# Kernel tuning notes

Hardware: AMD Instinct MI355X
Metric: run time of the kernel (lower is better)

The kernel has to match this reference:

```python
import jax, jax.numpy as jnp
import numpy as np

B, P, K = 32, 1024, 16  # clouds, points per cloud, neighbors


def setup_inputs() -> dict:
    key = jax.random.key(0)
    ks = jax.random.split(key, 5)
    N, C, H, D = B * P, 64, 128, 3
    x = jax.random.normal(ks[0], (N, C), dtype=jnp.float32)
    pos = jax.random.normal(ks[1], (N, D), dtype=jnp.float32)
    batch = jnp.arange(N, dtype=jnp.int64) // P  # cloud id per node
    W_e = jax.random.normal(ks[2], (2 * C, H), dtype=jnp.float32) * 0.05
    b_e = jnp.zeros((H,), dtype=jnp.float32)
    W_sc = jax.random.normal(ks[3], (C, H), dtype=jnp.float32) * 0.05
    b_sc = jnp.zeros((H,), dtype=jnp.float32)
    return {"x": x, "pos": pos, "batch": batch,
            "W_e": W_e, "b_e": b_e, "W_sc": W_sc, "b_sc": b_sc}


def _knn_idx(posb):
    # posb: [B, P, D] -> idx [B, P, K]: K nearest neighbors (sources) per target node,
    # within each cloud, excluding self (loop=False in torch_geometric.knn_graph).
    sq = jnp.sum(posb * posb, axis=-1)                       # [B, P]
    d2 = sq[:, :, None] + sq[:, None, :] - 2.0 * jnp.einsum('bid,bjd->bij', posb, posb)
    d2 = d2 + jnp.eye(P, dtype=posb.dtype)[None] * jnp.finfo(posb.dtype).max / 2
    _, idx = jax.lax.top_k(-d2, K)                           # [B, P, K]
    return idx


def reference(x, pos, batch, W_e, b_e, W_sc, b_sc):
    C = x.shape[-1]
    xb = x.reshape(B, P, C)
    posb = pos.reshape(B, P, -1)
    idx = _knn_idx(posb)                                     # [B, P, K]
    # gather neighbor (source) features per target node
    x_j = jax.vmap(lambda xc, ic: xc[ic])(xb, idx)           # [B, P, K, C]
    x_i = xb[:, :, None, :]                                  # [B, P, 1, C]
    # EdgeConv message: nn([x_i, x_j - x_i]), here Linear + ReLU
    e = jnp.concatenate([jnp.broadcast_to(x_i, x_j.shape), x_j - x_i], axis=-1)  # [B,P,K,2C]
    msg = jax.nn.relu(jnp.einsum('bpke,eh->bpkh', e, W_e) + b_e)
    agg = jnp.max(msg, axis=2)                               # max aggregation -> [B, P, H]
    shortcut = x @ W_sc + b_sc                               # [N, H]
    out = agg.reshape(-1, agg.shape[-1]) + shortcut
    return out
```

## Files before the change

### kernel.cpp

```cpp
#include <hip/hip_runtime.h>
#include <float.h>
#include <stdint.h>

#define BATCHES 32
#define P 1024
#define KNN 16
#define C 64
#define H 128
#define N (BATCHES * P)
#define NCOLS 384
#define SPLITS 8
#define CPS 128
#define PADH 132

typedef short short8 __attribute__((ext_vector_type(8)));
typedef float floatx4 __attribute__((ext_vector_type(4)));

__device__ __forceinline__ unsigned short f2bf(float f) {
    unsigned u = __float_as_uint(f);
    unsigned r = (u + 0x7FFF + ((u >> 16) & 1)) >> 16;
    return (unsigned short)r;
}

__global__ __launch_bounds__(256) void prep_w(
    const float* __restrict__ W_e, const float* __restrict__ b_e,
    const float* __restrict__ W_sc, const float* __restrict__ b_sc,
    unsigned short* __restrict__ WT, float* __restrict__ bias)
{
    int i = blockIdx.x * 256 + threadIdx.x;
    int col = i >> 6, c = i & 63;
    float w;
    if (col < 128)      w = W_e[c * 128 + col] - W_e[(64 + c) * 128 + col];
    else if (col < 256) w = W_e[(64 + c) * 128 + (col - 128)];
    else                w = W_sc[c * 128 + (col - 256)];
    WT[col * 64 + c] = f2bf(w);
    if (c == 0) {
        bias[col] = (col < 128) ? b_e[col] : (col < 256 ? 0.0f : b_sc[col - 256]);
    }
}

struct alignas(16) F4 { float x, y, z, w; };

struct PA {
    F4    spos[P];
    float lists[SPLITS][16][64];
    unsigned short elist[SPLITS][16][64];
    int   ecnt[SPLITS][64];
    float Tq[64];
};
struct PB {
    unsigned short Ubuf[64][PADH];
    unsigned short Vbuf[64][PADH];
    unsigned short Sbuf[64][PADH];
};

__global__ __launch_bounds__(512) void knn_gemm_kernel(
    const float* __restrict__ pos, const float* __restrict__ X,
    const unsigned short* __restrict__ WT, const float* __restrict__ bias,
    int* __restrict__ idx_out,
    unsigned short* __restrict__ U, unsigned short* __restrict__ V,
    unsigned short* __restrict__ S)
{
    __shared__ __align__(16) char smraw[sizeof(PA)];
    PA* A  = (PA*)smraw;
    PB* Bm = (PB*)smraw;

    int t = threadIdx.x;
    int q = t & 63, s = t >> 6;
    int blk = blockIdx.x;
    int batch = blk >> 4;
    int qblk  = blk & 15;
    int iloc  = qblk * 64 + q;

    const float* pb = pos + (size_t)batch * P * 3;
    for (int j = t; j < P; j += 512) {
        float x = pb[j * 3 + 0], y = pb[j * 3 + 1], z = pb[j * 3 + 2];
        float sq = __fadd_rn(__fadd_rn(__fmul_rn(x, x), __fmul_rn(y, y)),
                             __fmul_rn(z, z));
        A->spos[j] = F4{x, y, z, sq};
    }
    __syncthreads();

    F4 me = A->spos[iloc];
    float d[16];
#pragma unroll
    for (int k = 0; k < 16; ++k) d[k] = FLT_MAX;

    const int j0 = s * CPS;
#pragma unroll 4
    for (int jj = 0; jj < CPS; ++jj) {
        int j = j0 + jj;
        F4 c = A->spos[j];
        float dot = __fadd_rn(__fadd_rn(__fmul_rn(me.x, c.x), __fmul_rn(me.y, c.y)),
                              __fmul_rn(me.z, c.z));
        float d2 = __fadd_rn(__fadd_rn(me.w, c.w), __fmul_rn(-2.0f, dot));
        if (j == iloc) d2 = FLT_MAX;
#pragma unroll
        for (int k = 15; k >= 1; --k)
            d[k] = __builtin_amdgcn_fmed3f(d[k - 1], d2, d[k]);
        d[0] = fminf(d[0], d2);
    }
#pragma unroll
    for (int k = 0; k < 16; ++k) A->lists[s][k][q] = d[k];
    __syncthreads();

    if (s == 0) {
        float v0 = A->lists[0][0][q], v1 = A->lists[1][0][q];
        float v2 = A->lists[2][0][q], v3 = A->lists[3][0][q];
        float v4 = A->lists[4][0][q], v5 = A->lists[5][0][q];
        float v6 = A->lists[6][0][q], v7 = A->lists[7][0][q];
        int p0 = 0, p1 = 0, p2 = 0, p3 = 0, p4 = 0, p5 = 0, p6 = 0, p7 = 0;
        float T = 0.0f;
        for (int k = 0; k < 16; ++k) {
            float mn = fminf(fminf(fminf(v0, v1), fminf(v2, v3)),
                             fminf(fminf(v4, v5), fminf(v6, v7)));
            if      (v0 == mn) { p0++; v0 = (p0 < 16) ? A->lists[0][p0][q] : FLT_MAX; }
            else if (v1 == mn) { p1++; v1 = (p1 < 16) ? A->lists[1][p1][q] : FLT_MAX; }
            else if (v2 == mn) { p2++; v2 = (p2 < 16) ? A->lists[2][p2][q] : FLT_MAX; }
            else if (v3 == mn) { p3++; v3 = (p3 < 16) ? A->lists[3][p3][q] : FLT_MAX; }
            else if (v4 == mn) { p4++; v4 = (p4 < 16) ? A->lists[4][p4][q] : FLT_MAX; }
            else if (v5 == mn) { p5++; v5 = (p5 < 16) ? A->lists[5][p5][q] : FLT_MAX; }
            else if (v6 == mn) { p6++; v6 = (p6 < 16) ? A->lists[6][p6][q] : FLT_MAX; }
            else               { p7++; v7 = (p7 < 16) ? A->lists[7][p7][q] : FLT_MAX; }
            T = mn;
        }
        A->Tq[q] = T;
    }
    __syncthreads();
    float T = A->Tq[q];

    int cnt = 0;
    for (int jj = 0; jj < CPS; ++jj) {
        int j = j0 + jj;
        F4 c = A->spos[j];
        float dot = __fadd_rn(__fadd_rn(__fmul_rn(me.x, c.x), __fmul_rn(me.y, c.y)),
                              __fmul_rn(me.z, c.z));
        float d2 = __fadd_rn(__fadd_rn(me.w, c.w), __fmul_rn(-2.0f, dot));
        if (j == iloc) d2 = FLT_MAX;
        if (d2 <= T && cnt < 16) {
            A->elist[s][cnt][q] = (unsigned short)j;
            cnt++;
        }
    }
    A->ecnt[s][q] = cnt;
    __syncthreads();

    if (s == 0) {
        int o = 0;
        int base = batch * P;
        int gbase = (blk * 64 + q) * KNN;
#pragma unroll
        for (int ss = 0; ss < SPLITS; ++ss) {
            int cc = A->ecnt[ss][q];
            for (int k = 0; k < cc && o < KNN; ++k) {
                idx_out[gbase + o] = base + (int)A->elist[ss][k][q];
                o++;
            }
        }
    }
    __syncthreads();

    {
        int mt = s & 3, nh = s >> 2;
        int m0 = blk * 64 + mt * 16;
        int lm = q & 15, kg = q >> 4;

        const float4* arow = (const float4*)(X + (size_t)(m0 + lm) * 64 + kg * 8);
        float4 f0 = arow[0], f1 = arow[1];
        float4 f2 = arow[8], f3 = arow[9];
        short8 a0, a1;
        a0[0] = (short)f2bf(f0.x); a0[1] = (short)f2bf(f0.y);
        a0[2] = (short)f2bf(f0.z); a0[3] = (short)f2bf(f0.w);
        a0[4] = (short)f2bf(f1.x); a0[5] = (short)f2bf(f1.y);
        a0[6] = (short)f2bf(f1.z); a0[7] = (short)f2bf(f1.w);
        a1[0] = (short)f2bf(f2.x); a1[1] = (short)f2bf(f2.y);
        a1[2] = (short)f2bf(f2.z); a1[3] = (short)f2bf(f2.w);
        a1[4] = (short)f2bf(f3.x); a1[5] = (short)f2bf(f3.y);
        a1[6] = (short)f2bf(f3.z); a1[7] = (short)f2bf(f3.w);

#pragma unroll 4
        for (int nt = nh * 12; nt < nh * 12 + 12; ++nt) {
            const short8* brow = (const short8*)(WT + (size_t)(nt * 16 + lm) * 64 + kg * 8);
            short8 b0 = brow[0];
            short8 b1 = brow[4];
            floatx4 acc = {0.0f, 0.0f, 0.0f, 0.0f};
            acc = __builtin_amdgcn_mfma_f32_16x16x32_bf16(a0, b0, acc, 0, 0, 0);
            acc = __builtin_amdgcn_mfma_f32_16x16x32_bf16(a1, b1, acc, 0, 0, 0);

            int col = nt * 16 + lm;
            float bv = bias[col];
#pragma unroll
            for (int r = 0; r < 4; ++r) {
                int row = mt * 16 + kg * 4 + r;
                unsigned short val = f2bf(acc[r] + bv);
                if (col < 128)      Bm->Ubuf[row][col] = val;
                else if (col < 256) Bm->Vbuf[row][col - 128] = val;
                else                Bm->Sbuf[row][col - 256] = val;
            }
        }
    }
    __syncthreads();

    {
        uint2* Ug = (uint2*)U + (size_t)blk * 2048;
        uint2* Vg = (uint2*)V + (size_t)blk * 2048;
        uint2* Sg = (uint2*)S + (size_t)blk * 2048;
#pragma unroll
        for (int i = t; i < 2048; i += 512) {
            int row = i >> 5, off = (i & 31) * 4;
            Ug[i] = *(const uint2*)&Bm->Ubuf[row][off];
            Vg[i] = *(const uint2*)&Bm->Vbuf[row][off];
            Sg[i] = *(const uint2*)&Bm->Sbuf[row][off];
        }
    }
}

__global__ __launch_bounds__(256) void final_kernel(
    const int* __restrict__ idx, const unsigned short* __restrict__ U,
    const unsigned short* __restrict__ V, const unsigned short* __restrict__ S,
    float* __restrict__ out)
{
    int t = threadIdx.x;
    __shared__ int nbr[8][KNN];
    if (t < 128) ((int*)nbr)[t] = idx[(size_t)blockIdx.x * 128 + t];
    __syncthreads();

    int w = t >> 6, l = t & 63;
    int half = l >> 5, c4 = l & 31;
    int pl = w * 2 + half;
    size_t p = (size_t)blockIdx.x * 8 + pl;

    uint2 uu = ((const uint2*)(U + p * H))[c4];
    uint2 ss = ((const uint2*)(S + p * H))[c4];

    float m0 = -FLT_MAX, m1 = -FLT_MAX, m2 = -FLT_MAX, m3 = -FLT_MAX;
#pragma unroll
    for (int k = 0; k < KNN; ++k) {
        int row = nbr[pl][k];
        uint2 vv = *(const uint2*)(V + (size_t)row * H + c4 * 4);
        m0 = fmaxf(m0, __uint_as_float(vv.x << 16));
        m1 = fmaxf(m1, __uint_as_float(vv.x & 0xFFFF0000u));
        m2 = fmaxf(m2, __uint_as_float(vv.y << 16));
        m3 = fmaxf(m3, __uint_as_float(vv.y & 0xFFFF0000u));
    }

    float4 o;
    o.x = fmaxf(__uint_as_float(uu.x << 16)          + m0, 0.0f) + __uint_as_float(ss.x << 16);
    o.y = fmaxf(__uint_as_float(uu.x & 0xFFFF0000u)  + m1, 0.0f) + __uint_as_float(ss.x & 0xFFFF0000u);
    o.z = fmaxf(__uint_as_float(uu.y << 16)          + m2, 0.0f) + __uint_as_float(ss.y << 16);
    o.w = fmaxf(__uint_as_float(uu.y & 0xFFFF0000u)  + m3, 0.0f) + __uint_as_float(ss.y & 0xFFFF0000u);
    ((float4*)(out + p * H))[c4] = o;
}

extern "C" void kernel_launch(void* const* d_in, const int* in_sizes, int n_in,
                              void* d_out, int out_size, void* d_ws, size_t ws_size,
                              hipStream_t stream)
{
    const float* x    = (const float*)d_in[0];
    const float* pos  = (const float*)d_in[1];
    const float* W_e  = (const float*)d_in[3];
    const float* b_e  = (const float*)d_in[4];
    const float* W_sc = (const float*)d_in[5];
    const float* b_sc = (const float*)d_in[6];
    float* out = (float*)d_out;

    char* ws = (char*)d_ws;
    const size_t OFF_IDX  = 0;
    const size_t OFF_U    = 2ull << 20;
    const size_t OFF_V    = OFF_U + (8ull << 20);
    const size_t OFF_S    = OFF_V + (8ull << 20);
    const size_t OFF_WT   = OFF_S + (8ull << 20);
    const size_t OFF_BIAS = OFF_WT + 49152;

    int*            idx  = (int*)(ws + OFF_IDX);
    unsigned short* U    = (unsigned short*)(ws + OFF_U);
    unsigned short* V    = (unsigned short*)(ws + OFF_V);
    unsigned short* S    = (unsigned short*)(ws + OFF_S);
    unsigned short* WT   = (unsigned short*)(ws + OFF_WT);
    float*          bias = (float*)(ws + OFF_BIAS);

    prep_w<<<(NCOLS * C) / 256, 256, 0, stream>>>(W_e, b_e, W_sc, b_sc, WT, bias);
    knn_gemm_kernel<<<512, 512, 0, stream>>>(pos, x, WT, bias, idx, U, V, S);
    final_kernel<<<N / 8, 256, 0, stream>>>(idx, U, V, S, out);
}
```

Measured before the change: 145.0 us.

## Write kNN indices directly from each split using merge-derived per-split counts

```diff
diff --git a/kernel.cpp b/kernel.cpp
--- a/kernel.cpp
+++ b/kernel.cpp
@@ -42,10 +42,10 @@
 struct alignas(16) F4 { float x, y, z, w; };
 
 struct PA {
-    F4    spos[P];
+    F4    spos[P + 8];
     float lists[SPLITS][16][64];
-    unsigned short elist[SPLITS][16][64];
-    int   ecnt[SPLITS][64];
+    unsigned short offs[SPLITS][64];
+    unsigned short cnts[SPLITS][64];
     float Tq[64];
 };
 struct PB {
@@ -82,23 +82,40 @@
     __syncthreads();
 
     F4 me = A->spos[iloc];
+    const int j0 = s * CPS;
+
     float d[16];
 #pragma unroll
     for (int k = 0; k < 16; ++k) d[k] = FLT_MAX;
 
-    const int j0 = s * CPS;
-#pragma unroll 4
-    for (int jj = 0; jj < CPS; ++jj) {
-        int j = j0 + jj;
-        F4 c = A->spos[j];
+    auto dist = [&](const F4& c, int j) -> float {
         float dot = __fadd_rn(__fadd_rn(__fmul_rn(me.x, c.x), __fmul_rn(me.y, c.y)),
                               __fmul_rn(me.z, c.z));
         float d2 = __fadd_rn(__fadd_rn(me.w, c.w), __fmul_rn(-2.0f, dot));
-        if (j == iloc) d2 = FLT_MAX;
+        return (j == iloc) ? FLT_MAX : d2;
+    };
+    auto insert = [&](float d2) {
 #pragma unroll
         for (int k = 15; k >= 1; --k)
             d[k] = __builtin_amdgcn_fmed3f(d[k - 1], d2, d[k]);
         d[0] = fminf(d[0], d2);
+    };
+
+    {
+        F4 c0 = A->spos[j0 + 0], c1 = A->spos[j0 + 1];
+        F4 c2 = A->spos[j0 + 2], c3 = A->spos[j0 + 3];
+#pragma unroll 2
+        for (int jj = 0; jj < CPS; jj += 4) {
+            F4 n0 = A->spos[j0 + jj + 4];
+            F4 n1 = A->spos[j0 + jj + 5];
+            F4 n2 = A->spos[j0 + jj + 6];
+            F4 n3 = A->spos[j0 + jj + 7];
+            insert(dist(c0, j0 + jj + 0));
+            insert(dist(c1, j0 + jj + 1));
+            insert(dist(c2, j0 + jj + 2));
+            insert(dist(c3, j0 + jj + 3));
+            c0 = n0; c1 = n1; c2 = n2; c3 = n3;
+        }
     }
 #pragma unroll
     for (int k = 0; k < 16; ++k) A->lists[s][k][q] = d[k];
@@ -109,53 +126,65 @@
         float v2 = A->lists[2][0][q], v3 = A->lists[3][0][q];
         float v4 = A->lists[4][0][q], v5 = A->lists[5][0][q];
         float v6 = A->lists[6][0][q], v7 = A->lists[7][0][q];
-        int p0 = 0, p1 = 0, p2 = 0, p3 = 0, p4 = 0, p5 = 0, p6 = 0, p7 = 0;
+        float w0 = A->lists[0][1][q], w1 = A->lists[1][1][q];
+        float w2 = A->lists[2][1][q], w3 = A->lists[3][1][q];
+        float w4 = A->lists[4][1][q], w5 = A->lists[5][1][q];
+        float w6 = A->lists[6][1][q], w7 = A->lists[7][1][q];
+        int n0 = 0, n1 = 0, n2 = 0, n3 = 0, n4 = 0, n5 = 0, n6 = 0, n7 = 0;
         float T = 0.0f;
+#pragma unroll 1
         for (int k = 0; k < 16; ++k) {
             float mn = fminf(fminf(fminf(v0, v1), fminf(v2, v3)),
                              fminf(fminf(v4, v5), fminf(v6, v7)));
-            if      (v0 == mn) { p0++; v0 = (p0 < 16) ? A->lists[0][p0][q] : FLT_MAX; }
-            else if (v1 == mn) { p1++; v1 = (p1 < 16) ? A->lists[1][p1][q] : FLT_MAX; }
-            else if (v2 == mn) { p2++; v2 = (p2 < 16) ? A->lists[2][p2][q] : FLT_MAX; }
-            else if (v3 == mn) { p3++; v3 = (p3 < 16) ? A->lists[3][p3][q] : FLT_MAX; }
-            else if (v4 == mn) { p4++; v4 = (p4 < 16) ? A->lists[4][p4][q] : FLT_MAX; }
-            else if (v5 == mn) { p5++; v5 = (p5 < 16) ? A->lists[5][p5][q] : FLT_MAX; }
-            else if (v6 == mn) { p6++; v6 = (p6 < 16) ? A->lists[6][p6][q] : FLT_MAX; }
-            else               { p7++; v7 = (p7 < 16) ? A->lists[7][p7][q] : FLT_MAX; }
+            if      (v0 == mn) { n0++; v0 = w0; w0 = (n0 + 1 < 16) ? A->lists[0][n0 + 1][q] : FLT_MAX; }
+            else if (v1 == mn) { n1++; v1 = w1; w1 = (n1 + 1 < 16) ? A->lists[1][n1 + 1][q] : FLT_MAX; }
+            else if (v2 == mn) { n2++; v2 = w2; w2 = (n2 + 1 < 16) ? A->lists[2][n2 + 1][q] : FLT_MAX; }
+            else if (v3 == mn) { n3++; v3 = w3; w3 = (n3 + 1 < 16) ? A->lists[3][n3 + 1][q] : FLT_MAX; }
+            else if (v4 == mn) { n4++; v4 = w4; w4 = (n4 + 1 < 16) ? A->lists[4][n4 + 1][q] : FLT_MAX; }
+            else if (v5 == mn) { n5++; v5 = w5; w5 = (n5 + 1 < 16) ? A->lists[5][n5 + 1][q] : FLT_MAX; }
+            else if (v6 == mn) { n6++; v6 = w6; w6 = (n6 + 1 < 16) ? A->lists[6][n6 + 1][q] : FLT_MAX; }
+            else               { n7++; v7 = w7; w7 = (n7 + 1 < 16) ? A->lists[7][n7 + 1][q] : FLT_MAX; }
             T = mn;
         }
         A->Tq[q] = T;
-    }
-    __syncthreads();
-    float T = A->Tq[q];
-
-    int cnt = 0;
-    for (int jj = 0; jj < CPS; ++jj) {
-        int j = j0 + jj;
-        F4 c = A->spos[j];
-        float dot = __fadd_rn(__fadd_rn(__fmul_rn(me.x, c.x), __fmul_rn(me.y, c.y)),
-                              __fmul_rn(me.z, c.z));
-        float d2 = __fadd_rn(__fadd_rn(me.w, c.w), __fmul_rn(-2.0f, dot));
-        if (j == iloc) d2 = FLT_MAX;
-        if (d2 <= T && cnt < 16) {
-            A->elist[s][cnt][q] = (unsigned short)j;
-            cnt++;
-        }
-    }
-    A->ecnt[s][q] = cnt;
-    __syncthreads();
-
-    if (s == 0) {
-        int o = 0;
-        int base = batch * P;
-        int gbase = (blk * 64 + q) * KNN;
-#pragma unroll
-        for (int ss = 0; ss < SPLITS; ++ss) {
-            int cc = A->ecnt[ss][q];
-            for (int k = 0; k < cc && o < KNN; ++k) {
-                idx_out[gbase + o] = base + (int)A->elist[ss][k][q];
-                o++;
+        int off = 0;
+        A->offs[0][q] = (unsigned short)off; A->cnts[0][q] = (unsigned short)n0; off += n0;
+        A->offs[1][q] = (unsigned short)off; A->cnts[1][q] = (unsigned short)n1; off += n1;
+        A->offs[2][q] = (unsigned short)off; A->cnts[2][q] = (unsigned short)n2; off += n2;
+        A->offs[3][q] = (unsigned short)off; A->cnts[3][q] = (unsigned short)n3; off += n3;
+        A->offs[4][q] = (unsigned short)off; A->cnts[4][q] = (unsigned short)n4; off += n4;
+        A->offs[5][q] = (unsigned short)off; A->cnts[5][q] = (unsigned short)n5; off += n5;
+        A->offs[6][q] = (unsigned short)off; A->cnts[6][q] = (unsigned short)n6; off += n6;
+        A->offs[7][q] = (unsigned short)off; A->cnts[7][q] = (unsigned short)n7;
+    }
+    __syncthreads();
+
+    {
+        float T  = A->Tq[q];
+        int   cap = A->cnts[s][q];
+        int   gb  = ((blk << 6) + q) * KNN + A->offs[s][q];
+        int   base = batch * P;
+        int   cnt = 0;
+
+        F4 c0 = A->spos[j0 + 0], c1 = A->spos[j0 + 1];
+        F4 c2 = A->spos[j0 + 2], c3 = A->spos[j0 + 3];
+#pragma unroll 2
+        for (int jj = 0; jj < CPS; jj += 4) {
+            F4 n0 = A->spos[j0 + jj + 4];
+            F4 n1 = A->spos[j0 + jj + 5];
+            F4 n2 = A->spos[j0 + jj + 6];
+            F4 n3 = A->spos[j0 + jj + 7];
+#pragma unroll
+            for (int u = 0; u < 4; ++u) {
+                const F4& c = (u == 0) ? c0 : (u == 1) ? c1 : (u == 2) ? c2 : c3;
+                int j = j0 + jj + u;
+                float d2 = dist(c, j);
+                if (d2 <= T && cnt < cap) {
+                    idx_out[gb + cnt] = base + j;
+                    cnt++;
+                }
             }
+            c0 = n0; c1 = n1; c2 = n2; c3 = n3;
         }
     }
     __syncthreads();
```

After: 144.2 us. Within noise of the previous version (-0.6%).
